# Kernel optimization log

Hardware: AMD Instinct MI355X
Metric: run time of the kernel (lower is better)

Reference implementation:

```python
import jax, jax.numpy as jnp
import numpy as np
from jax.scipy.special import erfinv

EMBED = 384
HEADS = 6
HEAD_DIM = EMBED // HEADS  # 64
N_FREQS = HEAD_DIM // 2    # 32
SEQ = 1025                 # 1 CLS + 32*32 patches
POS_DIM = 2
MIN_FREQ, MAX_FREQ = 0.1, 1000.0


def _phi(m: int) -> float:
    x = 2.0
    for _ in range(10):
        x = (1.0 + x) ** (1.0 / (m + 1.0))
    return x


def _uniform_directions(n: int, d: int) -> jnp.ndarray:
    # golden-ratio quasi-random directions, normalized (matches uniform_directions_jax)
    g = _phi(d)
    alpha = (1.0 / g) ** jnp.arange(1, d + 1, dtype=jnp.float32)
    i = jnp.arange(1, n + 1, dtype=jnp.float32)[:, None]
    z = jnp.fmod(i * alpha, 1.0)
    dirs = erfinv(2.0 * z - 1.0)
    return dirs / jnp.linalg.norm(dirs, axis=1, keepdims=True)


def _rope_freqs() -> jnp.ndarray:  # [h, F, P]
    omega = MIN_FREQ * (MAX_FREQ / MIN_FREQ) ** jnp.linspace(0.0, 1.0, N_FREQS)
    dirs = _uniform_directions(HEADS * N_FREQS, POS_DIM).reshape(HEADS, N_FREQS, POS_DIM)
    return dirs * omega.reshape(1, N_FREQS, 1)


def _coords_2d() -> jnp.ndarray:  # [S, 2], CLS at origin, patches in [-1,1]^2
    n = int(np.sqrt(SEQ - 1))  # 32
    yy, xx = jnp.meshgrid(jnp.arange(n), jnp.arange(n), indexing='ij')
    xf = xx.flatten().astype(jnp.float32) / (n - 1) * 2 - 1
    yf = yy.flatten().astype(jnp.float32) / (n - 1) * 2 - 1
    patch = jnp.stack([xf, yf], axis=1)
    return jnp.concatenate([jnp.zeros((1, 2), jnp.float32), patch], axis=0)


def _apply_rope(t_bshd, freqs_hFP, coords_SP):
    # theta: [S, h, F]
    theta = jnp.einsum('hfp,sp->shf', freqs_hFP, coords_SP)
    cos, sin = jnp.cos(theta), jnp.sin(theta)  # broadcast over batch
    x1, y1 = jnp.split(t_bshd, 2, axis=-1)     # [b,s,h,F] each
    return jnp.concatenate([x1 * cos - y1 * sin, x1 * sin + y1 * cos], axis=-1)


def setup_inputs() -> dict:
    key = jax.random.key(0)
    ks = jax.random.split(key, 6)
    scale = 1.0 / np.sqrt(EMBED)
    return {
        'x':  jax.random.normal(ks[0], (16, SEQ, EMBED), jnp.float32),
        'Wq': jax.random.normal(ks[1], (EMBED, EMBED), jnp.float32) * scale,
        'Wk': jax.random.normal(ks[2], (EMBED, EMBED), jnp.float32) * scale,
        'Wv': jax.random.normal(ks[3], (EMBED, EMBED), jnp.float32) * scale,
        'Wo': jax.random.normal(ks[4], (EMBED, EMBED), jnp.float32) * scale,
        'bo': jnp.zeros((EMBED,), jnp.float32),
    }


def reference(x, Wq, Wk, Wv, Wo, bo):
    b, s, e = x.shape
    freqs = _rope_freqs()   # constant buffers
    coords = _coords_2d()
    q = (x @ Wq).reshape(b, s, HEADS, HEAD_DIM)
    k = (x @ Wk).reshape(b, s, HEADS, HEAD_DIM)
    v = (x @ Wv).reshape(b, s, HEADS, HEAD_DIM)
    q = _apply_rope(q, freqs, coords)
    k = _apply_rope(k, freqs, coords)
    scores = jnp.einsum('blhd,bmhd->bhlm', q, k) / np.sqrt(HEAD_DIM)
    attn = jax.nn.softmax(scores, axis=-1)
    out = jnp.einsum('bhlm,bmhd->blhd', attn, v).reshape(b, s, e)
    return out @ Wo + bo
```

## Files before the change

### kernel.cpp

```cpp
#include <hip/hip_runtime.h>
#include <hip/hip_bf16.h>
#include <math.h>

#define EMBED 384
#define HEADS 6
#define HD    64
#define NF    32
#define SEQ   1025
#define SEQP  1088
#define BATCH 16
#define MTOT  (BATCH*SEQ)
#define NCHUNK 17
#define LSTRIDE 72
#define VSTR   68

#define NB_X2B 6150
#define NB_TW  144
#define NB_RT  769

typedef __bf16 bf16x8 __attribute__((ext_vector_type(8)));
typedef __bf16 bf16x4 __attribute__((ext_vector_type(4)));
typedef float  f32x4  __attribute__((ext_vector_type(4)));
typedef short  s16x4  __attribute__((ext_vector_type(4)));

#define MFMA_BF16(A,B,C) __builtin_amdgcn_mfma_f32_16x16x32_bf16((A),(B),(C),0,0,0)
#define MFMA16(A,B,C) __builtin_amdgcn_mfma_f32_16x16x16bf16_1k((A),(B),(C),0,0,0)

#define GLL16(gp, lp) __builtin_amdgcn_global_load_lds( \
    (const __attribute__((address_space(1))) void*)(gp), \
    (__attribute__((address_space(3))) void*)(lp), 16, 0, 0)

__device__ __forceinline__ __bf16 f2bf(float f){
    __hip_bfloat16 h = __float2bfloat16(f);
    return *reinterpret_cast<__bf16*>(&h);
}
__device__ __forceinline__ short bfbits(float f){
    __hip_bfloat16 h = __float2bfloat16(f);
    return *reinterpret_cast<short*>(&h);
}

__device__ __forceinline__ float erfinv_f(float x){
    float w = -log1pf(-x*x);
    float p;
    if (w < 5.0f){
        w -= 2.5f;
        p = 2.81022636e-08f;
        p = fmaf(p, w, 3.43273939e-07f);
        p = fmaf(p, w, -3.5233877e-06f);
        p = fmaf(p, w, -4.39150654e-06f);
        p = fmaf(p, w, 0.00021858087f);
        p = fmaf(p, w, -0.00125372503f);
        p = fmaf(p, w, -0.00417768164f);
        p = fmaf(p, w, 0.246640727f);
        p = fmaf(p, w, 1.50140941f);
    } else {
        w = sqrtf(w) - 3.0f;
        p = -0.000200214257f;
        p = fmaf(p, w, 0.000100950558f);
        p = fmaf(p, w, 0.00134934322f);
        p = fmaf(p, w, -0.00367342844f);
        p = fmaf(p, w, 0.00573950773f);
        p = fmaf(p, w, -0.0076224613f);
        p = fmaf(p, w, 0.00943887047f);
        p = fmaf(p, w, 1.00167406f);
        p = fmaf(p, w, 2.83297682f);
    }
    return p * x;
}

__global__ __launch_bounds__(256) void prep_kernel(
    const float* __restrict__ x, __hip_bfloat16* __restrict__ xb,
    const float* __restrict__ Wq, const float* __restrict__ Wk,
    const float* __restrict__ Wv, const float* __restrict__ Wo,
    __hip_bfloat16* __restrict__ Wt,
    float* __restrict__ cos_t, float* __restrict__ sin_t)
{
    __shared__ float tile[64][65];
    const int bid = blockIdx.x;
    const int tid = threadIdx.x;

    if (bid < NB_X2B){
        int i = bid*256 + tid;
        float4 v = *reinterpret_cast<const float4*>(x + (size_t)i*4);
        bf16x4 b; b[0]=f2bf(v.x); b[1]=f2bf(v.y); b[2]=f2bf(v.z); b[3]=f2bf(v.w);
        *reinterpret_cast<bf16x4*>(reinterpret_cast<__bf16*>(xb) + (size_t)i*4) = b;
        return;
    }
    if (bid < NB_X2B + NB_TW){
        int idx = bid - NB_X2B;
        const int mat = idx / 36;
        const int rem = idx % 36;
        const int kx = rem / 6, ny = rem % 6;
        const float* W = (mat==0)?Wq:(mat==1)?Wk:(mat==2)?Wv:Wo;
        const int k0 = kx*64, n0 = ny*64;
        const int c = tid & 63, rq = tid >> 6;
        #pragma unroll
        for (int i = 0; i < 16; ++i){
            int row = rq*16 + i;
            tile[row][c] = W[(size_t)(k0+row)*EMBED + n0 + c];
        }
        __syncthreads();
        #pragma unroll
        for (int i = 0; i < 16; ++i){
            int nr = rq*16 + i;
            Wt[((size_t)mat*EMBED + n0 + nr)*EMBED + k0 + c] = __float2bfloat16(tile[c][nr]);
        }
        return;
    }
    int idx = (bid - NB_X2B - NB_TW)*256 + tid;
    if (idx >= SEQ*HEADS*NF) return;
    int f  = idx & (NF-1);
    int hf = idx / NF;
    int h  = hf % HEADS;
    int s  = hf / HEADS;

    double xd = 2.0;
    #pragma unroll
    for (int it = 0; it < 10; ++it) xd = cbrt(1.0 + xd);
    float a1 = (float)(1.0 / xd);
    float a2 = a1 * a1;

    float fi = (float)(h*NF + f + 1);
    float z1 = fmodf(fi * a1, 1.0f);
    float z2 = fmodf(fi * a2, 1.0f);
    float d1 = erfinv_f(2.0f*z1 - 1.0f);
    float d2 = erfinv_f(2.0f*z2 - 1.0f);
    float inv = 1.0f / sqrtf(d1*d1 + d2*d2);
    d1 *= inv; d2 *= inv;

    float omega = 0.1f * powf(10000.0f, (float)f / 31.0f);
    float fx = d1 * omega, fy = d2 * omega;

    float cx = 0.0f, cy = 0.0f;
    if (s > 0){
        int pi = s - 1;
        cx = (float)(pi & 31) / 31.0f * 2.0f - 1.0f;
        cy = (float)(pi >> 5) / 31.0f * 2.0f - 1.0f;
    }
    float theta = fx*cx + fy*cy;
    float sv, cv;
    sincosf(theta, &sv, &cv);
    cos_t[idx] = cv;
    sin_t[idx] = sv;
}

__global__ __launch_bounds__(256, 3) void qkv_rope_kernel(
    const __hip_bfloat16* __restrict__ xb_,
    const __hip_bfloat16* __restrict__ Wt,
    const float* __restrict__ cos_t,
    const float* __restrict__ sin_t,
    __hip_bfloat16* __restrict__ qbuf,
    __hip_bfloat16* __restrict__ kbuf,
    __hip_bfloat16* __restrict__ vbuf)
{
    __shared__ __align__(16) __bf16 xs[128*32];
    __shared__ __align__(16) __bf16 bt[128*32];
    const int tid = threadIdx.x;
    const int m0 = blockIdx.x * 128;
    const int j  = blockIdx.y;
    const __bf16* xb = reinterpret_cast<const __bf16*>(xb_);
    const __bf16* wt = reinterpret_cast<const __bf16*>(Wt);

    const int w = tid >> 6;
    const int lane = tid & 63;
    const int quad = lane >> 4, low = lane & 15;
    const int rg = lane >> 2, cg = lane & 3;

    int arow[2], brow[2], loff[2];
    #pragma unroll
    for (int i = 0; i < 2; ++i){
        int row = (w*2 + i)*16 + rg;
        int am = m0 + row; if (am > MTOT-1) am = MTOT-1;
        arow[i] = am;
        brow[i] = j*128 + row;
        loff[i] = (w*2 + i)*1024;
    }

    const int mh = w >> 1, nh = w & 1;
    const int mw0 = m0 + mh*64;

    f32x4 acc[4][4] = {};
    for (int kb = 0; kb < 12; ++kb){
        const int kc = kb*32;
        __syncthreads();
        #pragma unroll
        for (int i = 0; i < 2; ++i){
            GLL16(xb + (size_t)arow[i]*EMBED + kc + cg*8, (char*)xs + loff[i]);
            GLL16(wt + (size_t)brow[i]*EMBED + kc + cg*8, (char*)bt + loff[i]);
        }
        __syncthreads();
        bf16x8 af[4], bfr[4];
        #pragma unroll
        for (int mt = 0; mt < 4; ++mt)
            af[mt] = *reinterpret_cast<const bf16x8*>(&xs[(mh*64 + mt*16 + low)*32 + quad*8]);
        #pragma unroll
        for (int t = 0; t < 4; ++t)
            bfr[t] = *reinterpret_cast<const bf16x8*>(&bt[(nh*64 + t*16 + low)*32 + quad*8]);
        #pragma unroll
        for (int t = 0; t < 4; ++t)
            #pragma unroll
            for (int mt = 0; mt < 4; ++mt)
                acc[mt][t] = MFMA_BF16(af[mt], bfr[t], acc[mt][t]);
    }

    const int n64 = j*2 + nh;
    const int mat = n64 / 6;
    const int h   = n64 % 6;

    if (mat == 2){
        #pragma unroll
        for (int mt = 0; mt < 4; ++mt)
            #pragma unroll
            for (int t = 0; t < 4; ++t)
                #pragma unroll
                for (int r = 0; r < 4; ++r){
                    int m = mw0 + mt*16 + quad*4 + r;
                    if (m < MTOT){
                        int b = m / SEQ, s = m % SEQ;
                        vbuf[((size_t)(b*HEADS + h)*SEQ + s)*HD + t*16 + low] = __float2bfloat16(acc[mt][t][r]);
                    }
                }
    } else {
        __hip_bfloat16* ob = (mat == 0) ? qbuf : kbuf;
        const float qs_ = (mat == 0) ? 0.125f : 1.0f;
        #pragma unroll
        for (int mt = 0; mt < 4; ++mt)
            #pragma unroll
            for (int t = 0; t < 2; ++t)
                #pragma unroll
                for (int r = 0; r < 4; ++r){
                    int m = mw0 + mt*16 + quad*4 + r;
                    if (m < MTOT){
                        int b = m / SEQ, s = m % SEQ;
                        int f = t*16 + low;
                        float cv = cos_t[(s*HEADS + h)*NF + f];
                        float sv = sin_t[(s*HEADS + h)*NF + f];
                        float x1 = acc[mt][t][r];
                        float y1 = acc[mt][t+2][r];
                        size_t base = ((size_t)(b*HEADS + h)*SEQ + s)*HD;
                        ob[base + f]      = __float2bfloat16((x1*cv - y1*sv)*qs_);
                        ob[base + NF + f] = __float2bfloat16((x1*sv + y1*cv)*qs_);
                    }
                }
    }
}

__global__ __launch_bounds__(256) void vt_transpose_kernel(
    const __hip_bfloat16* __restrict__ v, __hip_bfloat16* __restrict__ vt)
{
    __shared__ __bf16 tileT[64*72];
    const int tid = threadIdx.x;
    const int bh = blockIdx.x;
    const int s0 = blockIdx.y * 64;
    const __bf16* vb = reinterpret_cast<const __bf16*>(v) + (size_t)bh*SEQ*HD;
    #pragma unroll
    for (int i = 0; i < 2; ++i){
        int ch = tid + i*256;
        int srow = ch >> 3, dg = ch & 7;
        int s = s0 + srow; if (s > SEQ-1) s = SEQ-1;
        bf16x8 val = *reinterpret_cast<const bf16x8*>(vb + (size_t)s*HD + dg*8);
        #pragma unroll
        for (int e = 0; e < 8; ++e)
            tileT[(dg*8 + e)*72 + srow] = val[e];
    }
    __syncthreads();
    __bf16* ot = reinterpret_cast<__bf16*>(vt) + (size_t)bh*HD*SEQP;
    #pragma unroll
    for (int i = 0; i < 2; ++i){
        int ch = tid + i*256;
        int d = ch >> 3, sg = ch & 7;
        bf16x8 val = *reinterpret_cast<const bf16x8*>(&tileT[d*72 + sg*8]);
        *reinterpret_cast<bf16x8*>(ot + (size_t)d*SEQP + s0 + sg*8) = val;
    }
}

__global__ __launch_bounds__(256, 4) void attn_kernel(
    const __hip_bfloat16* __restrict__ qbuf,
    const __hip_bfloat16* __restrict__ kbuf,
    const __hip_bfloat16* __restrict__ vtbuf,
    __hip_bfloat16* __restrict__ aout)
{
    __shared__ __align__(16) __bf16 kls[64*LSTRIDE];
    __shared__ __align__(16) __bf16 vls[64*VSTR];
    const int tid  = threadIdx.x;
    const int w    = tid >> 6;
    const int lane = tid & 63;
    const int quad = lane >> 4, low = lane & 15;
    const int id = blockIdx.x;
    const int bh = id % 96;
    const int qt = id / 96;
    const int b = bh / HEADS, h = bh % HEADS;
    const __bf16* qb = reinterpret_cast<const __bf16*>(qbuf);
    const __bf16* kb = reinterpret_cast<const __bf16*>(kbuf);
    const __bf16* vt = reinterpret_cast<const __bf16*>(vtbuf);
    const size_t base   = (size_t)bh * SEQ * HD;
    const size_t vtbase = (size_t)bh * HD * SEQP;
    const int q0 = qt*128 + w*32;

    int srow[2], sgk[2], soffk[2], soffv[2];
    #pragma unroll
    for (int i = 0; i < 2; ++i){
        int ch = tid + i*256;
        srow[i] = ch >> 3; sgk[i] = ch & 7;
        soffk[i] = srow[i]*LSTRIDE + sgk[i]*8;
        soffv[i] = srow[i]*VSTR    + sgk[i]*8;
    }

    bf16x8 bq[2][2];
    #pragma unroll
    for (int nt = 0; nt < 2; ++nt){
        int qs = q0 + nt*16 + low; if (qs > SEQ-1) qs = SEQ-1;
        #pragma unroll
        for (int ks = 0; ks < 2; ++ks)
            bq[nt][ks] = *reinterpret_cast<const bf16x8*>(qb + base + (size_t)qs*HD + ks*32 + quad*8);
    }

    bf16x8 kr[2], vr[2];
    #pragma unroll
    for (int i = 0; i < 2; ++i){
        int kk = srow[i]; if (kk > SEQ-1) kk = SEQ-1;
        kr[i] = *reinterpret_cast<const bf16x8*>(kb + base + (size_t)kk*HD + sgk[i]*8);
        vr[i] = *reinterpret_cast<const bf16x8*>(vt + vtbase + (size_t)srow[i]*SEQP + sgk[i]*8);
    }

    f32x4 o[2][4] = {};
    float l_i[2] = {0.f, 0.f};

    for (int c = 0; c < NCHUNK; ++c){
        const int c0 = c*64;
        __syncthreads();
        #pragma unroll
        for (int i = 0; i < 2; ++i){
            *reinterpret_cast<bf16x8*>(&kls[soffk[i]]) = kr[i];
            bf16x4 vlo = __builtin_shufflevector(vr[i], vr[i], 0,1,2,3);
            bf16x4 vhi = __builtin_shufflevector(vr[i], vr[i], 4,5,6,7);
            *reinterpret_cast<bf16x4*>(&vls[soffv[i]])     = vlo;
            *reinterpret_cast<bf16x4*>(&vls[soffv[i] + 4]) = vhi;
        }
        __syncthreads();
        if (c + 1 < NCHUNK){
            const int c1 = c0 + 64;
            #pragma unroll
            for (int i = 0; i < 2; ++i){
                int kk = c1 + srow[i]; if (kk > SEQ-1) kk = SEQ-1;
                kr[i] = *reinterpret_cast<const bf16x8*>(kb + base + (size_t)kk*HD + sgk[i]*8);
                vr[i] = *reinterpret_cast<const bf16x8*>(vt + vtbase + (size_t)srow[i]*SEQP + c1 + sgk[i]*8);
            }
        }
        f32x4 st[4][2] = {};
        #pragma unroll
        for (int kt = 0; kt < 4; ++kt)
            #pragma unroll
            for (int ks = 0; ks < 2; ++ks){
                bf16x8 ak = *reinterpret_cast<const bf16x8*>(&kls[(kt*16 + low)*LSTRIDE + ks*32 + quad*8]);
                #pragma unroll
                for (int nt = 0; nt < 2; ++nt)
                    st[kt][nt] = MFMA_BF16(ak, bq[nt][ks], st[kt][nt]);
            }
        if (c0 + 64 > SEQ){
            #pragma unroll
            for (int kt = 0; kt < 4; ++kt)
                #pragma unroll
                for (int r = 0; r < 4; ++r){
                    int key = c0 + kt*16 + quad*4 + r;
                    if (key >= SEQ){ st[kt][0][r] = -1e30f; st[kt][1][r] = -1e30f; }
                }
        }
        s16x4 pa[4][2];
        #pragma unroll
        for (int nt = 0; nt < 2; ++nt)
            #pragma unroll
            for (int kt = 0; kt < 4; ++kt)
                #pragma unroll
                for (int r = 0; r < 4; ++r){
                    float p = __expf(st[kt][nt][r]);
                    l_i[nt] += p;
                    pa[kt][nt][r] = bfbits(p);
                }
        #pragma unroll
        for (int kt = 0; kt < 4; ++kt)
            #pragma unroll
            for (int dt = 0; dt < 4; ++dt){
                const s16x4 bv = *reinterpret_cast<const s16x4*>(&vls[(dt*16 + low)*VSTR + kt*16 + quad*4]);
                #pragma unroll
                for (int nt = 0; nt < 2; ++nt)
                    o[nt][dt] = MFMA16(pa[kt][nt], bv, o[nt][dt]);
            }
    }

    #pragma unroll
    for (int nt = 0; nt < 2; ++nt){
        l_i[nt] += __shfl_xor(l_i[nt], 16, 64);
        l_i[nt] += __shfl_xor(l_i[nt], 32, 64);
    }
    float lq[2][4];
    #pragma unroll
    for (int nt = 0; nt < 2; ++nt)
        #pragma unroll
        for (int r = 0; r < 4; ++r)
            lq[nt][r] = __shfl(l_i[nt], quad*4 + r, 64);

    #pragma unroll
    for (int nt = 0; nt < 2; ++nt)
        #pragma unroll
        for (int r = 0; r < 4; ++r){
            int s = q0 + nt*16 + quad*4 + r;
            if (s < SEQ){
                float inv = 1.0f / lq[nt][r];
                __hip_bfloat16* dst = aout + ((size_t)b*SEQ + s)*EMBED + h*HD;
                #pragma unroll
                for (int dt = 0; dt < 4; ++dt)
                    dst[dt*16 + low] = __float2bfloat16(o[nt][dt][r]*inv);
            }
        }
}

__global__ __launch_bounds__(128) void outproj_kernel(
    const __hip_bfloat16* __restrict__ a,
    const __hip_bfloat16* __restrict__ Wt,
    const float* __restrict__ bo,
    float* __restrict__ out)
{
    __shared__ __align__(16) __bf16 xs[64*32];
    __shared__ __align__(16) __bf16 bt[128*32];
    const int tid = threadIdx.x;
    const int m0 = blockIdx.x * 64;
    const int j  = blockIdx.y;
    const __bf16* ab = reinterpret_cast<const __bf16*>(a);
    const __bf16* wt = reinterpret_cast<const __bf16*>(Wt) + (size_t)3*EMBED*EMBED;

    const int w = tid >> 6;
    const int lane = tid & 63;
    const int quad = lane >> 4, low = lane & 15;
    const int rg = lane >> 2, cg = lane & 3;

    int arow[2], aoff[2];
    #pragma unroll
    for (int i = 0; i < 2; ++i){
        int row = (w*2 + i)*16 + rg;
        int am = m0 + row; if (am > MTOT-1) am = MTOT-1;
        arow[i] = am;
        aoff[i] = (w*2 + i)*1024;
    }
    int brow[4], boff[4];
    #pragma unroll
    for (int i = 0; i < 4; ++i){
        int row = (w*4 + i)*16 + rg;
        brow[i] = j*128 + row;
        boff[i] = (w*4 + i)*1024;
    }

    f32x4 acc[4][4] = {};
    for (int kb = 0; kb < 12; ++kb){
        const int kc = kb*32;
        __syncthreads();
        #pragma unroll
        for (int i = 0; i < 2; ++i)
            GLL16(ab + (size_t)arow[i]*EMBED + kc + cg*8, (char*)xs + aoff[i]);
        #pragma unroll
        for (int i = 0; i < 4; ++i)
            GLL16(wt + (size_t)brow[i]*EMBED + kc + cg*8, (char*)bt + boff[i]);
        __syncthreads();
        bf16x8 af[4], bfr[4];
        #pragma unroll
        for (int mt = 0; mt < 4; ++mt)
            af[mt] = *reinterpret_cast<const bf16x8*>(&xs[(mt*16 + low)*32 + quad*8]);
        #pragma unroll
        for (int t = 0; t < 4; ++t)
            bfr[t] = *reinterpret_cast<const bf16x8*>(&bt[(w*64 + t*16 + low)*32 + quad*8]);
        #pragma unroll
        for (int t = 0; t < 4; ++t)
            #pragma unroll
            for (int mt = 0; mt < 4; ++mt)
                acc[mt][t] = MFMA_BF16(af[mt], bfr[t], acc[mt][t]);
    }

    #pragma unroll
    for (int t = 0; t < 4; ++t){
        const int n = j*128 + w*64 + t*16 + low;
        const float bias = bo[n];
        #pragma unroll
        for (int mt = 0; mt < 4; ++mt)
            #pragma unroll
            for (int r = 0; r < 4; ++r){
                const int m = m0 + mt*16 + quad*4 + r;
                if (m < MTOT) out[(size_t)m*EMBED + n] = acc[mt][t][r] + bias;
            }
    }
}

extern "C" void kernel_launch(void* const* d_in, const int* in_sizes, int n_in,
                              void* d_out, int out_size, void* d_ws, size_t ws_size,
                              hipStream_t stream)
{
    const float* x  = (const float*)d_in[0];
    const float* Wq = (const float*)d_in[1];
    const float* Wk = (const float*)d_in[2];
    const float* Wv = (const float*)d_in[3];
    const float* Wo = (const float*)d_in[4];
    const float* bo = (const float*)d_in[5];
    float* out = (float*)d_out;

    const size_t NE = (size_t)MTOT * EMBED;
    const size_t VT = (size_t)BATCH*HEADS*HD*SEQP;
    char* ws = (char*)d_ws;
    size_t off = 0;
    __hip_bfloat16* qbuf = (__hip_bfloat16*)(ws + off); off += 2*NE;
    __hip_bfloat16* kbuf = (__hip_bfloat16*)(ws + off); off += 2*NE;
    __hip_bfloat16* abuf = (__hip_bfloat16*)(ws + off); off += 2*NE;
    __hip_bfloat16* vbuf = (__hip_bfloat16*)(ws + off); off += 2*NE;
    __hip_bfloat16* xbuf = (__hip_bfloat16*)(ws + off); off += 2*NE;
    __hip_bfloat16* vt   = (__hip_bfloat16*)(ws + off); off += 2*VT;
    __hip_bfloat16* Wt   = (__hip_bfloat16*)(ws + off); off += (size_t)4*EMBED*EMBED*2;
    float* cos_t = (float*)(ws + off); off += (size_t)SEQ*HEADS*NF*4;
    float* sin_t = (float*)(ws + off); off += (size_t)SEQ*HEADS*NF*4;

    prep_kernel<<<dim3(NB_X2B + NB_TW + NB_RT), dim3(256), 0, stream>>>(
        x, xbuf, Wq, Wk, Wv, Wo, Wt, cos_t, sin_t);
    qkv_rope_kernel<<<dim3((MTOT + 127)/128, 9), dim3(256), 0, stream>>>(xbuf, Wt, cos_t, sin_t, qbuf, kbuf, vbuf);
    vt_transpose_kernel<<<dim3(96, 17), dim3(256), 0, stream>>>(vbuf, vt);
    attn_kernel<<<dim3(864), dim3(256), 0, stream>>>(qbuf, kbuf, vt, abuf);
    outproj_kernel<<<dim3((MTOT + 63)/64, 3), dim3(128), 0, stream>>>(abuf, Wt, bo, out);
}
```

Measured before the change: 208.6 us.

## Double-buffer LDS tiles in QKV and output projection GEMMs

Both projection GEMM kernels now keep two LDS buffers for the A and B tiles. Each iteration issues the global-to-LDS loads for the next K chunk before running the MFMAs on the current one, which also cuts the barriers per iteration from two to one. The aim is to hide global load latency behind compute. The cost is doubled shared memory, which may lower occupancy. Correctness depends on the async LDS loads being waited on before the barrier.

```diff
diff --git a/kernel.cpp b/kernel.cpp
--- a/kernel.cpp
+++ b/kernel.cpp
@@ -153,8 +153,8 @@
     __hip_bfloat16* __restrict__ kbuf,
     __hip_bfloat16* __restrict__ vbuf)
 {
-    __shared__ __align__(16) __bf16 xs[128*32];
-    __shared__ __align__(16) __bf16 bt[128*32];
+    __shared__ __align__(16) __bf16 xs[2][128*32];
+    __shared__ __align__(16) __bf16 bt[2][128*32];
     const int tid = threadIdx.x;
     const int m0 = blockIdx.x * 128;
     const int j  = blockIdx.y;
@@ -176,31 +176,40 @@
         loff[i] = (w*2 + i)*1024;
     }
 
+    #pragma unroll
+    for (int i = 0; i < 2; ++i){
+        GLL16(xb + (size_t)arow[i]*EMBED + cg*8, (char*)xs[0] + loff[i]);
+        GLL16(wt + (size_t)brow[i]*EMBED + cg*8, (char*)bt[0] + loff[i]);
+    }
+    __syncthreads();
+
     const int mh = w >> 1, nh = w & 1;
     const int mw0 = m0 + mh*64;
 
     f32x4 acc[4][4] = {};
     for (int kb = 0; kb < 12; ++kb){
-        const int kc = kb*32;
-        __syncthreads();
-        #pragma unroll
-        for (int i = 0; i < 2; ++i){
-            GLL16(xb + (size_t)arow[i]*EMBED + kc + cg*8, (char*)xs + loff[i]);
-            GLL16(wt + (size_t)brow[i]*EMBED + kc + cg*8, (char*)bt + loff[i]);
-        }
-        __syncthreads();
+        const int cur = kb & 1;
+        if (kb < 11){
+            const int k1 = (kb+1)*32;
+            #pragma unroll
+            for (int i = 0; i < 2; ++i){
+                GLL16(xb + (size_t)arow[i]*EMBED + k1 + cg*8, (char*)xs[cur^1] + loff[i]);
+                GLL16(wt + (size_t)brow[i]*EMBED + k1 + cg*8, (char*)bt[cur^1] + loff[i]);
+            }
+        }
         bf16x8 af[4], bfr[4];
         #pragma unroll
         for (int mt = 0; mt < 4; ++mt)
-            af[mt] = *reinterpret_cast<const bf16x8*>(&xs[(mh*64 + mt*16 + low)*32 + quad*8]);
+            af[mt] = *reinterpret_cast<const bf16x8*>(&xs[cur][(mh*64 + mt*16 + low)*32 + quad*8]);
         #pragma unroll
         for (int t = 0; t < 4; ++t)
-            bfr[t] = *reinterpret_cast<const bf16x8*>(&bt[(nh*64 + t*16 + low)*32 + quad*8]);
+            bfr[t] = *reinterpret_cast<const bf16x8*>(&bt[cur][(nh*64 + t*16 + low)*32 + quad*8]);
         #pragma unroll
         for (int t = 0; t < 4; ++t)
             #pragma unroll
             for (int mt = 0; mt < 4; ++mt)
                 acc[mt][t] = MFMA_BF16(af[mt], bfr[t], acc[mt][t]);
+        if (kb < 11) __syncthreads();
     }
 
     const int n64 = j*2 + nh;
@@ -421,8 +430,8 @@
     const float* __restrict__ bo,
     float* __restrict__ out)
 {
-    __shared__ __align__(16) __bf16 xs[64*32];
-    __shared__ __align__(16) __bf16 bt[128*32];
+    __shared__ __align__(16) __bf16 xs[2][64*32];
+    __shared__ __align__(16) __bf16 bt[2][128*32];
     const int tid = threadIdx.x;
     const int m0 = blockIdx.x * 64;
     const int j  = blockIdx.y;
@@ -450,29 +459,39 @@
         boff[i] = (w*4 + i)*1024;
     }
 
+    #pragma unroll
+    for (int i = 0; i < 2; ++i)
+        GLL16(ab + (size_t)arow[i]*EMBED + cg*8, (char*)xs[0] + aoff[i]);
+    #pragma unroll
+    for (int i = 0; i < 4; ++i)
+        GLL16(wt + (size_t)brow[i]*EMBED + cg*8, (char*)bt[0] + boff[i]);
+    __syncthreads();
+
     f32x4 acc[4][4] = {};
     for (int kb = 0; kb < 12; ++kb){
-        const int kc = kb*32;
-        __syncthreads();
-        #pragma unroll
-        for (int i = 0; i < 2; ++i)
-            GLL16(ab + (size_t)arow[i]*EMBED + kc + cg*8, (char*)xs + aoff[i]);
-        #pragma unroll
-        for (int i = 0; i < 4; ++i)
-            GLL16(wt + (size_t)brow[i]*EMBED + kc + cg*8, (char*)bt + boff[i]);
-        __syncthreads();
+        const int cur = kb & 1;
+        if (kb < 11){
+            const int k1 = (kb+1)*32;
+            #pragma unroll
+            for (int i = 0; i < 2; ++i)
+                GLL16(ab + (size_t)arow[i]*EMBED + k1 + cg*8, (char*)xs[cur^1] + aoff[i]);
+            #pragma unroll
+            for (int i = 0; i < 4; ++i)
+                GLL16(wt + (size_t)brow[i]*EMBED + k1 + cg*8, (char*)bt[cur^1] + boff[i]);
+        }
         bf16x8 af[4], bfr[4];
         #pragma unroll
         for (int mt = 0; mt < 4; ++mt)
-            af[mt] = *reinterpret_cast<const bf16x8*>(&xs[(mt*16 + low)*32 + quad*8]);
+            af[mt] = *reinterpret_cast<const bf16x8*>(&xs[cur][(mt*16 + low)*32 + quad*8]);
         #pragma unroll
         for (int t = 0; t < 4; ++t)
-            bfr[t] = *reinterpret_cast<const bf16x8*>(&bt[(w*64 + t*16 + low)*32 + quad*8]);
+            bfr[t] = *reinterpret_cast<const bf16x8*>(&bt[cur][(w*64 + t*16 + low)*32 + quad*8]);
         #pragma unroll
         for (int t = 0; t < 4; ++t)
             #pragma unroll
             for (int mt = 0; mt < 4; ++mt)
                 acc[mt][t] = MFMA_BF16(af[mt], bfr[t], acc[mt][t]);
+        if (kb < 11) __syncthreads();
     }
 
     #pragma unroll
```

New measurement: 206.2 us. About the same (-1.1%).
